# Kernel optimization log

Hardware: AMD Instinct MI355X
Metric: run time of the kernel (lower is better)

The kernel has to match this reference:

```python
import jax, jax.numpy as jnp
import numpy as np

BOUND = 1.0
N_RAYS = 2048
TOT = 128        # num_steps (samples per pixel)
IND_S = 16       # indicator_steps
MAX_DEPTHS = 2
HID = 64
EPS = 1e-8


def setup_inputs() -> dict:
    key = jax.random.key(0)
    ks = jax.random.split(key, 13)
    M = N_RAYS * TOT
    rays_o = 0.3 * jax.random.normal(ks[0], (N_RAYS, 3), jnp.float32)
    rd = jax.random.normal(ks[1], (N_RAYS, 3), jnp.float32)
    rays_d = rd / (jnp.linalg.norm(rd, axis=-1, keepdims=True) + EPS)
    env_map = 0.1 * jax.random.normal(ks[2], (3, 128, 256), jnp.float32)
    Wd1 = jax.random.normal(ks[3], (3, HID), jnp.float32) / np.sqrt(3.0)
    Wd2 = jax.random.normal(ks[4], (HID, 3), jnp.float32) / np.sqrt(HID)
    Wf1 = jax.random.normal(ks[5], (6, HID), jnp.float32) / np.sqrt(6.0)
    Ws = jax.random.normal(ks[6], (HID, 3), jnp.float32) / np.sqrt(HID)
    Wdir = jax.random.normal(ks[7], (HID, 3), jnp.float32) / np.sqrt(HID)
    Wrho = jax.random.normal(ks[8], (HID, 3), jnp.float32) / np.sqrt(HID)
    jitter = jax.random.uniform(ks[9], (MAX_DEPTHS, M, IND_S), jnp.float32)
    u_t = jax.random.uniform(ks[10], (MAX_DEPTHS, M), jnp.float32)
    u_scatter = jax.random.uniform(ks[11], (MAX_DEPTHS, M), jnp.float32)
    channel = jax.random.randint(ks[12], (MAX_DEPTHS, M), 0, 3)
    return dict(rays_o=rays_o, rays_d=rays_d, env_map=env_map, Wd1=Wd1, Wd2=Wd2,
                Wf1=Wf1, Ws=Ws, Wdir=Wdir, Wrho=Wrho,
                jitter=jitter, u_t=u_t, u_scatter=u_scatter, channel=channel)


def _density(pts, Wd1, Wd2):
    # stand-in NeRF density field: 3 spectral channels, positive
    return jax.nn.softplus(jnp.sin(pts @ Wd1) @ Wd2)


def _material(o, d, Wf1, Ws, Wdir, Wrho):
    f = jnp.tanh(jnp.concatenate([o, d], axis=-1) @ Wf1)
    sigma_t = jax.nn.softplus(f @ Ws)                     # [M,3]
    dn = f @ Wdir
    d_out = dn / (jnp.linalg.norm(dn, axis=-1, keepdims=True) + EPS)
    fused_rho = jax.nn.sigmoid(f @ Wrho)                  # [M,3]
    return sigma_t, d_out, fused_rho


def _sample_env(env_map, p):
    # equirectangular lookup == torch grid_sample(bilinear, align_corners=False, zero pad)
    x, y, z = p[:, 0], p[:, 1], p[:, 2]
    theta = jnp.nan_to_num(jnp.arctan2(x, -z)) / jnp.pi            # grid x in [-1,1]
    phi = 2.0 / jnp.pi * jnp.nan_to_num(jnp.arccos(y)) - 1.0       # grid y in [-1,1]
    C, H, W = env_map.shape
    ix = ((theta + 1.0) * W - 1.0) * 0.5
    iy = ((phi + 1.0) * H - 1.0) * 0.5
    x0 = jnp.floor(ix); y0 = jnp.floor(iy)
    wx = ix - x0; wy = iy - y0

    def tap(xc, yc, w):
        inb = (xc >= 0) & (xc < W) & (yc >= 0) & (yc < H)
        xi = jnp.clip(xc, 0, W - 1).astype(jnp.int32)
        yi = jnp.clip(yc, 0, H - 1).astype(jnp.int32)
        return (w * inb)[:, None] * env_map[:, yi, xi].T   # [M,3]

    v = (tap(x0, y0, (1 - wx) * (1 - wy)) + tap(x0 + 1, y0, wx * (1 - wy)) +
         tap(x0, y0 + 1, (1 - wx) * wy) + tap(x0 + 1, y0 + 1, wx * wy))
    return jnp.exp(v)


def _render(rays_o, rays_d, env_map, Wd1, Wd2, Wf1, Ws, Wdir, Wrho,
            jitter, u_t, u_scatter, channel):
    M = N_RAYS * TOT
    o = jnp.repeat(rays_o, TOT, axis=0)   # [M,3]
    d = jnp.repeat(rays_d, TOT, axis=0)
    alive = jnp.ones((M,), bool)          # masked version of boolean compaction
    thr = jnp.ones((M, 3), jnp.float32)
    rgbs = jnp.zeros((M, 3), jnp.float32)
    lin = jnp.linspace(0.0, 1.0, IND_S)

    for dep in range(MAX_DEPTHS):
        # ray-sphere intersection (radius=bound)
        a = jnp.sum(d * d, -1)
        b = 2.0 * jnp.sum(d * o, -1)
        c = jnp.sum(o * o, -1) - BOUND ** 2
        delta = b * b - 4.0 * a * c
        alive = alive & (delta > 0.0)
        sq = jnp.sqrt(jnp.maximum(delta, 0.0))
        nears = jnp.maximum((-b - sq) / (2.0 * a), 0.001)
        fars = jnp.maximum((-b + sq) / (2.0 * a), 0.001)
        span = fars - nears

        # stratified indicator samples -> per-channel majorant
        z = nears[:, None] + span[:, None] * lin[None, :]
        z = z + (jitter[dep] - 0.5) * (span[:, None] / IND_S)
        pts = o[:, None, :] + d[:, None, :] * z[:, :, None]          # [M,S,3]
        sigma = _density(pts.reshape(-1, 3), Wd1, Wd2).reshape(M, IND_S, 3)
        ch = channel[dep]
        maj_multi = jnp.maximum(sigma.max(axis=1), 0.001)            # [M,3]
        sig_ch = jnp.take_along_axis(sigma, ch[:, None, None], axis=2)[..., 0]
        maj = jnp.maximum(sig_ch.max(axis=1), 0.001)                 # [M]

        # free-flight sampling (last depth forces hit at far boundary)
        if dep < MAX_DEPTHS - 1:
            t = -jnp.log1p(-u_t[dep]) / maj + nears
        else:
            t = fars
        hit = alive & (t >= fars)

        # environment hit contribution
        denom = jnp.exp(-maj_multi * span[:, None]) / (maj_multi.max(-1, keepdims=True) + EPS) + EPS
        Le = _sample_env(env_map, o + d * fars[:, None])
        contrib = thr * (denom / jax.lax.stop_gradient(denom.mean(-1, keepdims=True))) * Le
        rgbs = rgbs + jnp.where(hit[:, None], contrib, 0.0)
        alive = alive & ~hit
        if dep == MAX_DEPTHS - 1:
            break

        # throughput update + null/real scattering (delta tracking)
        trans = jnp.exp(-maj_multi * (t - nears)[:, None]) / maj_multi.max(-1, keepdims=True)
        den2 = jax.lax.stop_gradient((maj_multi * trans).mean(-1, keepdims=True))
        thr = jnp.where(alive[:, None], thr * trans / den2, thr)
        o = jnp.where(alive[:, None], jax.lax.stop_gradient(o + d * t[:, None]), o)
        sigma_t, d_out, fused_rho = _material(o, d, Wf1, Ws, Wdir, Wrho)
        sp = jnp.minimum(jnp.take_along_axis(sigma_t, ch[:, None], axis=1)[:, 0] / maj, 1.0)
        sm = alive & (u_scatter[dep] < sp)
        d = jnp.where(sm[:, None], d_out, d)
        thr = jnp.where(sm[:, None], thr / (sp[:, None] + EPS) * fused_rho,
              jnp.where(alive[:, None], thr / (1.0 - sp[:, None] + EPS), thr))

    return rgbs.reshape(N_RAYS, TOT, 3).mean(axis=1)   # [N,3]


def reference(rays_o, rays_d, env_map, Wd1, Wd2, Wf1, Ws, Wdir, Wrho,
              jitter, u_t, u_scatter, channel):
    return _render(rays_o, rays_d, env_map, Wd1, Wd2, Wf1, Ws, Wdir, Wrho,
                   jitter, u_t, u_scatter, channel)
```

## Files before the change

### kernel.cpp

```cpp
#include <hip/hip_runtime.h>
#include <math.h>

#define NRAYS 2048
#define TOT   128
#define INDS  16
#define HID   64
#define EPSF  1e-8f
#define MTOT  (NRAYS*TOT)
#define NTAB  128

typedef float f32x2 __attribute__((ext_vector_type(2)));
typedef float f32x4 __attribute__((ext_vector_type(4)));

__device__ __forceinline__ float softplus_f(float x) {
    return fmaxf(x, 0.0f) + __logf(1.0f + __expf(-fabsf(x)));
}
__device__ __forceinline__ float sigmoid_f(float x) {
    return 1.0f / (1.0f + __expf(-x));
}
__device__ __forceinline__ float tanh_fast(float x) {
    float e2 = __expf(2.0f * x);
    return 1.0f - 2.0f / (e2 + 1.0f);
}
__device__ __forceinline__ f32x2 pkmax(f32x2 a, f32x2 b) {
    f32x2 r; r.x = fmaxf(a.x, b.x); r.y = fmaxf(a.y, b.y); return r;
}
__device__ __forceinline__ f32x2 pkfma(f32x2 a, f32x2 b, f32x2 c) {
    return __builtin_elementwise_fma(a, b, c);
}
__device__ __forceinline__ f32x4 fma4(f32x4 a, f32x4 b, f32x4 c) {
    return __builtin_elementwise_fma(a, b, c);
}

#define CK(i) ((float)(i)*(1.0f/15.0f) - 0.03125f)

#define MAKE_Z(jA, jB, kbase, nears, span)                                    \
    float s16 = (span) * (1.0f/16.0f);                                        \
    f32x2 z01, z23, z45, z67;                                                 \
    z01.x = fmaf((jA).x, s16, fmaf(span, CK((kbase)+0), nears));              \
    z01.y = fmaf((jA).y, s16, fmaf(span, CK((kbase)+1), nears));              \
    z23.x = fmaf((jA).z, s16, fmaf(span, CK((kbase)+2), nears));              \
    z23.y = fmaf((jA).w, s16, fmaf(span, CK((kbase)+3), nears));              \
    z45.x = fmaf((jB).x, s16, fmaf(span, CK((kbase)+4), nears));              \
    z45.y = fmaf((jB).y, s16, fmaf(span, CK((kbase)+5), nears));              \
    z67.x = fmaf((jB).z, s16, fmaf(span, CK((kbase)+6), nears));              \
    z67.y = fmaf((jB).w, s16, fmaf(span, CK((kbase)+7), nears));

#define TAB_EVAL(zz, mx0, mx1, mx2)                                           \
    {                                                                         \
        float x = ((zz) - ztab0) * invh;                                      \
        x = fminf(fmaxf(x, 0.0f), (float)(NTAB-1) - 1e-3f);                   \
        int i = (int)x; float w = x - (float)i;                               \
        f32x4 Ta = sTab[i]; f32x4 Tb = sTab[i+1];                             \
        f32x4 wv = {w, w, w, w};                                              \
        f32x4 F = fma4(wv, Tb - Ta, Ta);                                      \
        mx0 = fmaxf(mx0, F.x); mx1 = fmaxf(mx1, F.y); mx2 = fmaxf(mx2, F.z);  \
    }

#define DENSITY_J_BODY(A2, B2, W0, W1, W2v)                                   \
    {                                                                         \
        f32x2 g01 = pkfma(z01, (B2), (A2));                                   \
        f32x2 g23 = pkfma(z23, (B2), (A2));                                   \
        f32x2 g45 = pkfma(z45, (B2), (A2));                                   \
        f32x2 g67 = pkfma(z67, (B2), (A2));                                   \
        f32x2 h01, h23, h45, h67;                                             \
        h01.x = __builtin_amdgcn_sinf(g01.x); h01.y = __builtin_amdgcn_sinf(g01.y); \
        h23.x = __builtin_amdgcn_sinf(g23.x); h23.y = __builtin_amdgcn_sinf(g23.y); \
        h45.x = __builtin_amdgcn_sinf(g45.x); h45.y = __builtin_amdgcn_sinf(g45.y); \
        h67.x = __builtin_amdgcn_sinf(g67.x); h67.y = __builtin_amdgcn_sinf(g67.y); \
        a0_01 = pkfma(h01,(W0),a0_01); a0_23 = pkfma(h23,(W0),a0_23);         \
        a0_45 = pkfma(h45,(W0),a0_45); a0_67 = pkfma(h67,(W0),a0_67);         \
        a1_01 = pkfma(h01,(W1),a1_01); a1_23 = pkfma(h23,(W1),a1_23);         \
        a1_45 = pkfma(h45,(W1),a1_45); a1_67 = pkfma(h67,(W1),a1_67);         \
        a2_01 = pkfma(h01,(W2v),a2_01); a2_23 = pkfma(h23,(W2v),a2_23);       \
        a2_45 = pkfma(h45,(W2v),a2_45); a2_67 = pkfma(h67,(W2v),a2_67);       \
    }

__device__ __forceinline__ void density_max3_half_d1(
    const f32x4* __restrict__ sPW, const f32x4* __restrict__ sW01,
    const f32x2* __restrict__ sW2,
    float ox, float oy, float oz, float dx, float dy, float dz,
    float nears, float span, float4 jA, float4 jB, int kbase,
    float& mx0o, float& mx1o, float& mx2o)
{
    MAKE_Z(jA, jB, kbase, nears, span)
    f32x2 a0_01 = {0.f,0.f}, a0_23 = {0.f,0.f}, a0_45 = {0.f,0.f}, a0_67 = {0.f,0.f};
    f32x2 a1_01 = {0.f,0.f}, a1_23 = {0.f,0.f}, a1_45 = {0.f,0.f}, a1_67 = {0.f,0.f};
    f32x2 a2_01 = {0.f,0.f}, a2_23 = {0.f,0.f}, a2_45 = {0.f,0.f}, a2_67 = {0.f,0.f};
    #pragma unroll 2
    for (int j = 0; j < HID; ++j) {
        f32x4 pw  = sPW[j];
        f32x4 w01 = sW01[j];
        f32x2 w2  = sW2[j];
        float A = fmaf(ox, pw.x, fmaf(oy, pw.y, oz*pw.z));
        float B = fmaf(dx, pw.x, fmaf(dy, pw.y, dz*pw.z));
        f32x2 A2 = {A, A}, B2 = {B, B};
        f32x2 W0 = {w01.x, w01.y}, W1 = {w01.z, w01.w};
        DENSITY_J_BODY(A2, B2, W0, W1, w2)
    }
    f32x2 p0 = pkmax(pkmax(a0_01, a0_23), pkmax(a0_45, a0_67));
    f32x2 p1 = pkmax(pkmax(a1_01, a1_23), pkmax(a1_45, a1_67));
    f32x2 p2 = pkmax(pkmax(a2_01, a2_23), pkmax(a2_45, a2_67));
    mx0o = fmaxf(p0.x, p0.y);
    mx1o = fmaxf(p1.x, p1.y);
    mx2o = fmaxf(p2.x, p2.y);
}

__device__ __forceinline__ void env_logv(
    const float* __restrict__ env_map,
    float px, float py, float pz,
    float& v0, float& v1, float& v2)
{
    float theta = atan2f(px, -pz) * (1.0f/3.14159265358979323846f);
    float acv = (fabsf(py) <= 1.0f) ? acosf(py) : 0.0f;
    float phi = 0.63661977236758134308f * acv - 1.0f;
    float ixf = ((theta + 1.0f)*256.0f - 1.0f)*0.5f;
    float iyf = ((phi   + 1.0f)*128.0f - 1.0f)*0.5f;
    float x0f = floorf(ixf), y0f = floorf(iyf);
    float wx = ixf - x0f, wy = iyf - y0f;
    v0 = 0.f; v1 = 0.f; v2 = 0.f;
    auto tap = [&](float xc, float yc, float w) {
        if (xc >= 0.0f && xc < 256.0f && yc >= 0.0f && yc < 128.0f) {
            int xi = (int)xc, yi = (int)yc;
            const float* e = env_map + yi*256 + xi;
            v0 += w * e[0];
            v1 += w * e[128*256];
            v2 += w * e[2*128*256];
        }
    };
    tap(x0f,      y0f,      (1.0f-wx)*(1.0f-wy));
    tap(x0f+1.0f, y0f,      wx*(1.0f-wy));
    tap(x0f,      y0f+1.0f, (1.0f-wx)*wy);
    tap(x0f+1.0f, y0f+1.0f, wx*wy);
}

__global__ __launch_bounds__(256)
void render_kernel(const float* __restrict__ rays_o,
                   const float* __restrict__ rays_d,
                   const float* __restrict__ env_map,
                   const float* __restrict__ Wd1,
                   const float* __restrict__ Wd2,
                   const float* __restrict__ Wf1,
                   const float* __restrict__ Ws,
                   const float* __restrict__ Wdir,
                   const float* __restrict__ Wrho,
                   const float* __restrict__ jitter,
                   const float* __restrict__ u_t,
                   const float* __restrict__ u_scatter,
                   const int*   __restrict__ channel,
                   float* __restrict__ out)
{
    const int ray  = blockIdx.x;
    const int tid  = threadIdx.x;
    const int s    = tid >> 1;
    const int half = tid & 1;
    const int m    = ray * TOT + s;
    const int kbase = half * 8;

    __shared__ f32x4 sAB[HID];
    __shared__ f32x4 sW01[HID];
    __shared__ f32x2 sW2[HID];
    __shared__ f32x4 sPW[HID];
    __shared__ f32x4 sM0[HID];
    __shared__ f32x4 sM1[HID];
    __shared__ f32x4 sM2[HID];
    __shared__ f32x4 sTab[NTAB];
    __shared__ f32x4 sP0[TOT];
    __shared__ f32x4 sP1[TOT];
    __shared__ f32x2 sP2[TOT];
    __shared__ float sEnvE[3];
    __shared__ int   sCnt;
    __shared__ float sred[4][3];

    const float4* j0p = (const float4*)(jitter + (size_t)m*INDS + kbase);
    const float4* j1p = (const float4*)(jitter + ((size_t)MTOT + m)*INDS + kbase);
    float4 j0A = j0p[0], j0B = j0p[1];
    float4 j1A = j1p[0], j1B = j1p[1];
    int   ch = channel[m];
    float ut = u_t[m];
    float us = u_scatter[m];

    float ox = rays_o[ray*3+0], oy = rays_o[ray*3+1], oz = rays_o[ray*3+2];
    float dx = rays_d[ray*3+0], dy = rays_d[ray*3+1], dz = rays_d[ray*3+2];

    if (tid == 0) sCnt = 0;
    if (tid < HID) {
        const float INV2PI = 0.15915494309189535f;
        float w1x = Wd1[tid], w1y = Wd1[HID+tid], w1z = Wd1[2*HID+tid];
        float pw1x = w1x*INV2PI, pw1y = w1y*INV2PI, pw1z = w1z*INV2PI;
        float A = ox*pw1x + oy*pw1y + oz*pw1z;
        float B = dx*pw1x + dy*pw1y + dz*pw1z;
        float w20 = Wd2[3*tid], w21 = Wd2[3*tid+1], w22 = Wd2[3*tid+2];
        sAB[tid]  = (f32x4){A, A, B, B};
        sW01[tid] = (f32x4){w20, w20, w21, w21};
        sW2[tid]  = (f32x2){w22, w22};
        sPW[tid]  = (f32x4){pw1x, pw1y, pw1z, 0.0f};
        float f0 = Wf1[tid],       f1 = Wf1[HID+tid],   f2 = Wf1[2*HID+tid];
        float f3 = Wf1[3*HID+tid], f4 = Wf1[4*HID+tid], f5 = Wf1[5*HID+tid];
        float P = ox*f0 + oy*f1 + oz*f2 + dx*f3 + dy*f4 + dz*f5;
        float Q = dx*f0 + dy*f1 + dz*f2;
        sM0[tid] = (f32x4){P, Q, Ws[3*tid], Ws[3*tid+1]};
        sM1[tid] = (f32x4){Ws[3*tid+2], Wdir[3*tid], Wdir[3*tid+1], Wdir[3*tid+2]};
        sM2[tid] = (f32x4){Wrho[3*tid], Wrho[3*tid+1], Wrho[3*tid+2], 0.0f};
    }
    __syncthreads();

    float a0g = dx*dx + dy*dy + dz*dz;
    float b0g = 2.0f*(dx*ox + dy*oy + dz*oz);
    float c0g = (ox*ox + oy*oy + oz*oz) - 1.0f;
    float delta0 = b0g*b0g - 4.0f*a0g*c0g;
    bool alive = (delta0 > 0.0f);

    float nears = 0.f, fars = 0.f, span = 0.f, ztab0 = 0.f, invh = 0.f;
    if (alive) {
        float sq = sqrtf(delta0);
        nears = fmaxf((-b0g - sq) / (2.0f*a0g), 0.001f);
        fars  = fmaxf((-b0g + sq) / (2.0f*a0g), 0.001f);
        span  = fars - nears;
        ztab0 = fmaf(-span, 0.03125f, nears);
        float width = span * 1.0625f;
        float hstep = width * (1.0f/(NTAB-1));
        invh = (float)(NTAB-1) / width;
        int p = tid >> 1;
        float zp = fmaf((float)p, hstep, ztab0);
        float f0 = 0.f, f1 = 0.f, f2 = 0.f;
        const int jb = half * 32;
        #pragma unroll 4
        for (int j = jb; j < jb + 32; ++j) {
            f32x4 ab  = sAB[j];
            f32x4 w01 = sW01[j];
            f32x2 w2  = sW2[j];
            float hv = __builtin_amdgcn_sinf(fmaf(zp, ab.z, ab.x));
            f0 = fmaf(hv, w01.x, f0);
            f1 = fmaf(hv, w01.z, f1);
            f2 = fmaf(hv, w2.x, f2);
        }
        f0 += __shfl_xor(f0, 1, 64);
        f1 += __shfl_xor(f1, 1, 64);
        f2 += __shfl_xor(f2, 1, 64);
        if (half == 0) sTab[p] = (f32x4){f0, f1, f2, 0.0f};
        if (tid == 0) {
            float v0,v1,v2;
            env_logv(env_map, fmaf(dx,fars,ox), fmaf(dy,fars,oy), fmaf(dz,fars,oz),
                     v0,v1,v2);
            sEnvE[0] = __expf(v0); sEnvE[1] = __expf(v1); sEnvE[2] = __expf(v2);
        }
    }
    __syncthreads();

    float thr0 = 1.f, thr1 = 1.f, thr2 = 1.f;
    float rgb0 = 0.f, rgb1 = 0.f, rgb2 = 0.f;
    bool  tab_d1 = false;
    float tadv = 0.f;

    if (alive) {
        MAKE_Z(j0A, j0B, kbase, nears, span)
        float mx0 = -1e30f, mx1 = -1e30f, mx2 = -1e30f;
        TAB_EVAL(z01.x, mx0,mx1,mx2) TAB_EVAL(z01.y, mx0,mx1,mx2)
        TAB_EVAL(z23.x, mx0,mx1,mx2) TAB_EVAL(z23.y, mx0,mx1,mx2)
        TAB_EVAL(z45.x, mx0,mx1,mx2) TAB_EVAL(z45.y, mx0,mx1,mx2)
        TAB_EVAL(z67.x, mx0,mx1,mx2) TAB_EVAL(z67.y, mx0,mx1,mx2)
        mx0 = fmaxf(mx0, __shfl_xor(mx0, 1, 64));
        mx1 = fmaxf(mx1, __shfl_xor(mx1, 1, 64));
        mx2 = fmaxf(mx2, __shfl_xor(mx2, 1, 64));

        float maj0 = fmaxf(softplus_f(mx0), 0.001f);
        float maj1 = fmaxf(softplus_f(mx1), 0.001f);
        float maj2 = fmaxf(softplus_f(mx2), 0.001f);
        float mmax = fmaxf(fmaxf(maj0, maj1), maj2);

        float maj = (ch == 0) ? maj0 : ((ch == 1) ? maj1 : maj2);
        float t   = -log1pf(-ut) / maj + nears;

        if (t >= fars) {
            float den0 = __expf(-maj0*span)/(mmax+EPSF) + EPSF;
            float den1 = __expf(-maj1*span)/(mmax+EPSF) + EPSF;
            float den2 = __expf(-maj2*span)/(mmax+EPSF) + EPSF;
            float idm = 3.0f / (den0+den1+den2);
            rgb0 = den0*idm*sEnvE[0];
            rgb1 = den1*idm*sEnvE[1];
            rgb2 = den2*idm*sEnvE[2];
        } else {
            float tn  = t - nears;
            float imm = 1.0f / mmax;
            float tr0 = __expf(-maj0*tn) * imm;
            float tr1 = __expf(-maj1*tn) * imm;
            float tr2 = __expf(-maj2*tn) * imm;
            float i2m = 3.0f / (maj0*tr0 + maj1*tr1 + maj2*tr2);
            thr0 = tr0 * i2m;
            thr1 = tr1 * i2m;
            thr2 = tr2 * i2m;
            ox = fmaf(dx, t, ox); oy = fmaf(dy, t, oy); oz = fmaf(dz, t, oz);

            float st0=0.f, st1=0.f, st2=0.f;
            float dn0=0.f, dn1=0.f, dn2v=0.f;
            float rh0=0.f, rh1=0.f, rh2=0.f;
            const int j0 = half * 32;
            #pragma unroll 2
            for (int j = j0; j < j0 + 32; ++j) {
                f32x4 q0 = sM0[j];
                f32x4 q1 = sM1[j];
                f32x4 q2 = sM2[j];
                float pre = fmaf(t, q0.y, q0.x);
                float f = tanh_fast(pre);
                st0  = fmaf(f, q0.z, st0);
                st1  = fmaf(f, q0.w, st1);
                st2  = fmaf(f, q1.x, st2);
                dn0  = fmaf(f, q1.y, dn0);
                dn1  = fmaf(f, q1.z, dn1);
                dn2v = fmaf(f, q1.w, dn2v);
                rh0  = fmaf(f, q2.x, rh0);
                rh1  = fmaf(f, q2.y, rh1);
                rh2  = fmaf(f, q2.z, rh2);
            }
            st0  += __shfl_xor(st0, 1, 64);
            st1  += __shfl_xor(st1, 1, 64);
            st2  += __shfl_xor(st2, 1, 64);
            dn0  += __shfl_xor(dn0, 1, 64);
            dn1  += __shfl_xor(dn1, 1, 64);
            dn2v += __shfl_xor(dn2v, 1, 64);
            rh0  += __shfl_xor(rh0, 1, 64);
            rh1  += __shfl_xor(rh1, 1, 64);
            rh2  += __shfl_xor(rh2, 1, 64);

            float stch = (ch == 0) ? st0 : ((ch == 1) ? st1 : st2);
            float sp = fminf(softplus_f(stch) / maj, 1.0f);
            if (us < sp) {
                float inr = 1.0f / (sqrtf(dn0*dn0 + dn1*dn1 + dn2v*dn2v) + EPSF);
                float ndx = dn0*inr, ndy = dn1*inr, ndz = dn2v*inr;
                float isp = 1.0f/(sp + EPSF);
                float t0 = thr0 * isp * sigmoid_f(rh0);
                float t1 = thr1 * isp * sigmoid_f(rh1);
                float t2 = thr2 * isp * sigmoid_f(rh2);
                if (half == 0) {
                    int sl = atomicAdd(&sCnt, 1);
                    sP0[sl] = (f32x4){ox, oy, oz, ndx};
                    sP1[sl] = (f32x4){ndy, ndz, t0, t1};
                    sP2[sl] = (f32x2){t2, (float)m};
                }
            } else {
                float iv = 1.0f/(1.0f - sp + EPSF);
                thr0 *= iv; thr1 *= iv; thr2 *= iv;
                tab_d1 = true;
                tadv = t;
            }
        }
    }
    __syncthreads();
    int npool = sCnt;

    if (tab_d1) {
        float a1 = dx*dx + dy*dy + dz*dz;
        float b1 = 2.0f*(dx*ox + dy*oy + dz*oz);
        float c1 = (ox*ox + oy*oy + oz*oz) - 1.0f;
        float delta1 = b1*b1 - 4.0f*a1*c1;
        if (delta1 > 0.0f) {
            float sq1    = sqrtf(delta1);
            float nears1 = fmaxf((-b1 - sq1) / (2.0f*a1), 0.001f);
            float fars1  = fmaxf((-b1 + sq1) / (2.0f*a1), 0.001f);
            float span1  = fars1 - nears1;
            MAKE_Z(j1A, j1B, kbase, nears1, span1)
            float mx0 = -1e30f, mx1 = -1e30f, mx2 = -1e30f;
            TAB_EVAL(tadv + z01.x, mx0,mx1,mx2) TAB_EVAL(tadv + z01.y, mx0,mx1,mx2)
            TAB_EVAL(tadv + z23.x, mx0,mx1,mx2) TAB_EVAL(tadv + z23.y, mx0,mx1,mx2)
            TAB_EVAL(tadv + z45.x, mx0,mx1,mx2) TAB_EVAL(tadv + z45.y, mx0,mx1,mx2)
            TAB_EVAL(tadv + z67.x, mx0,mx1,mx2) TAB_EVAL(tadv + z67.y, mx0,mx1,mx2)
            mx0 = fmaxf(mx0, __shfl_xor(mx0, 1, 64));
            mx1 = fmaxf(mx1, __shfl_xor(mx1, 1, 64));
            mx2 = fmaxf(mx2, __shfl_xor(mx2, 1, 64));

            float maj0 = fmaxf(softplus_f(mx0), 0.001f);
            float maj1 = fmaxf(softplus_f(mx1), 0.001f);
            float maj2 = fmaxf(softplus_f(mx2), 0.001f);
            float mmax = fmaxf(fmaxf(maj0, maj1), maj2);

            float den0 = __expf(-maj0*span1)/(mmax+EPSF) + EPSF;
            float den1 = __expf(-maj1*span1)/(mmax+EPSF) + EPSF;
            float den2 = __expf(-maj2*span1)/(mmax+EPSF) + EPSF;
            float idm = 3.0f / (den0+den1+den2);
            rgb0 += thr0 * den0*idm*sEnvE[0];
            rgb1 += thr1 * den1*idm*sEnvE[1];
            rgb2 += thr2 * den2*idm*sEnvE[2];
        }
    }

    {
        int q = tid >> 1;
        if (q < npool) {
            f32x4 p0 = sP0[q];
            f32x4 p1 = sP1[q];
            f32x2 p2 = sP2[q];
            float pox = p0.x, poy = p0.y, poz = p0.z;
            float pdx = p0.w, pdy = p1.x, pdz = p1.y;
            float pt0 = p1.z, pt1 = p1.w, pt2 = p2.x;
            int   mm  = (int)p2.y;
            const float4* jp = (const float4*)(jitter + ((size_t)MTOT + mm)*INDS + kbase);
            float4 jA = jp[0], jB = jp[1];

            float a1 = pdx*pdx + pdy*pdy + pdz*pdz;
            float b1 = 2.0f*(pdx*pox + pdy*poy + pdz*poz);
            float c1 = (pox*pox + poy*poy + poz*poz) - 1.0f;
            float delta1 = b1*b1 - 4.0f*a1*c1;
            if (delta1 > 0.0f) {
                float sq1    = sqrtf(delta1);
                float nears1 = fmaxf((-b1 - sq1) / (2.0f*a1), 0.001f);
                float fars1  = fmaxf((-b1 + sq1) / (2.0f*a1), 0.001f);
                float span1  = fars1 - nears1;

                float mx0, mx1, mx2;
                density_max3_half_d1(sPW, sW01, sW2, pox,poy,poz, pdx,pdy,pdz,
                                     nears1, span1, jA, jB, kbase, mx0,mx1,mx2);
                mx0 = fmaxf(mx0, __shfl_xor(mx0, 1, 64));
                mx1 = fmaxf(mx1, __shfl_xor(mx1, 1, 64));
                mx2 = fmaxf(mx2, __shfl_xor(mx2, 1, 64));

                float maj0 = fmaxf(softplus_f(mx0), 0.001f);
                float maj1 = fmaxf(softplus_f(mx1), 0.001f);
                float maj2 = fmaxf(softplus_f(mx2), 0.001f);
                float mmax = fmaxf(fmaxf(maj0, maj1), maj2);

                float den0 = __expf(-maj0*span1)/(mmax+EPSF) + EPSF;
                float den1 = __expf(-maj1*span1)/(mmax+EPSF) + EPSF;
                float den2 = __expf(-maj2*span1)/(mmax+EPSF) + EPSF;
                float idm = 3.0f / (den0+den1+den2);
                float v0,v1,v2;
                env_logv(env_map, fmaf(pdx,fars1,pox), fmaf(pdy,fars1,poy),
                         fmaf(pdz,fars1,poz), v0,v1,v2);
                rgb0 += pt0 * den0*idm*__expf(v0);
                rgb1 += pt1 * den1*idm*__expf(v1);
                rgb2 += pt2 * den2*idm*__expf(v2);
            }
        }
    }

    float r0 = rgb0, r1 = rgb1, r2 = rgb2;
    #pragma unroll
    for (int off = 32; off > 0; off >>= 1) {
        r0 += __shfl_down(r0, off, 64);
        r1 += __shfl_down(r1, off, 64);
        r2 += __shfl_down(r2, off, 64);
    }
    int wave = tid >> 6;
    if ((tid & 63) == 0) {
        sred[wave][0] = r0; sred[wave][1] = r1; sred[wave][2] = r2;
    }
    __syncthreads();
    if (tid == 0) {
        out[ray*3+0] = (sred[0][0]+sred[1][0]+sred[2][0]+sred[3][0]) * (1.0f/256.0f);
        out[ray*3+1] = (sred[0][1]+sred[1][1]+sred[2][1]+sred[3][1]) * (1.0f/256.0f);
        out[ray*3+2] = (sred[0][2]+sred[1][2]+sred[2][2]+sred[3][2]) * (1.0f/256.0f);
    }
}

extern "C" void kernel_launch(void* const* d_in, const int* in_sizes, int n_in,
                              void* d_out, int out_size, void* d_ws, size_t ws_size,
                              hipStream_t stream) {
    const float* rays_o    = (const float*)d_in[0];
    const float* rays_d    = (const float*)d_in[1];
    const float* env_map   = (const float*)d_in[2];
    const float* Wd1       = (const float*)d_in[3];
    const float* Wd2       = (const float*)d_in[4];
    const float* Wf1       = (const float*)d_in[5];
    const float* Ws        = (const float*)d_in[6];
    const float* Wdir      = (const float*)d_in[7];
    const float* Wrho      = (const float*)d_in[8];
    const float* jitter    = (const float*)d_in[9];
    const float* u_t       = (const float*)d_in[10];
    const float* u_scatter = (const float*)d_in[11];
    const int*   channel   = (const int*)d_in[12];
    float* out = (float*)d_out;

    render_kernel<<<dim3(NRAYS), dim3(256), 0, stream>>>(
        rays_o, rays_d, env_map, Wd1, Wd2, Wf1, Ws, Wdir, Wrho,
        jitter, u_t, u_scatter, channel, out);
}
```

Before: 168.1 us.

## Split pooled depth-1 density eval across four lanes per sample with strided loop

The pooled second-bounce density evaluation now assigns each compacted sample to four lanes, each handling four indicator steps instead of eight. A strided loop covers the whole pool, and a second xor-shuffle stage combines the four partial maxima. The depth-1 jitter load moves inside the branch that needs it, so rays that miss the sphere skip it. This shortens the serial sine and FMA chain per lane and balances work across the block. The cost is more shuffles, duplicated env lookups across lanes, and loop overhead when the pool exceeds 64 samples.

New measurement: 168.3 us. Within noise of the previous version (+0.2%).

```diff
diff --git a/kernel.cpp b/kernel.cpp
--- a/kernel.cpp
+++ b/kernel.cpp
@@ -56,55 +56,6 @@
         f32x4 F = fma4(wv, Tb - Ta, Ta);                                      \
         mx0 = fmaxf(mx0, F.x); mx1 = fmaxf(mx1, F.y); mx2 = fmaxf(mx2, F.z);  \
     }
-
-#define DENSITY_J_BODY(A2, B2, W0, W1, W2v)                                   \
-    {                                                                         \
-        f32x2 g01 = pkfma(z01, (B2), (A2));                                   \
-        f32x2 g23 = pkfma(z23, (B2), (A2));                                   \
-        f32x2 g45 = pkfma(z45, (B2), (A2));                                   \
-        f32x2 g67 = pkfma(z67, (B2), (A2));                                   \
-        f32x2 h01, h23, h45, h67;                                             \
-        h01.x = __builtin_amdgcn_sinf(g01.x); h01.y = __builtin_amdgcn_sinf(g01.y); \
-        h23.x = __builtin_amdgcn_sinf(g23.x); h23.y = __builtin_amdgcn_sinf(g23.y); \
-        h45.x = __builtin_amdgcn_sinf(g45.x); h45.y = __builtin_amdgcn_sinf(g45.y); \
-        h67.x = __builtin_amdgcn_sinf(g67.x); h67.y = __builtin_amdgcn_sinf(g67.y); \
-        a0_01 = pkfma(h01,(W0),a0_01); a0_23 = pkfma(h23,(W0),a0_23);         \
-        a0_45 = pkfma(h45,(W0),a0_45); a0_67 = pkfma(h67,(W0),a0_67);         \
-        a1_01 = pkfma(h01,(W1),a1_01); a1_23 = pkfma(h23,(W1),a1_23);         \
-        a1_45 = pkfma(h45,(W1),a1_45); a1_67 = pkfma(h67,(W1),a1_67);         \
-        a2_01 = pkfma(h01,(W2v),a2_01); a2_23 = pkfma(h23,(W2v),a2_23);       \
-        a2_45 = pkfma(h45,(W2v),a2_45); a2_67 = pkfma(h67,(W2v),a2_67);       \
-    }
-
-__device__ __forceinline__ void density_max3_half_d1(
-    const f32x4* __restrict__ sPW, const f32x4* __restrict__ sW01,
-    const f32x2* __restrict__ sW2,
-    float ox, float oy, float oz, float dx, float dy, float dz,
-    float nears, float span, float4 jA, float4 jB, int kbase,
-    float& mx0o, float& mx1o, float& mx2o)
-{
-    MAKE_Z(jA, jB, kbase, nears, span)
-    f32x2 a0_01 = {0.f,0.f}, a0_23 = {0.f,0.f}, a0_45 = {0.f,0.f}, a0_67 = {0.f,0.f};
-    f32x2 a1_01 = {0.f,0.f}, a1_23 = {0.f,0.f}, a1_45 = {0.f,0.f}, a1_67 = {0.f,0.f};
-    f32x2 a2_01 = {0.f,0.f}, a2_23 = {0.f,0.f}, a2_45 = {0.f,0.f}, a2_67 = {0.f,0.f};
-    #pragma unroll 2
-    for (int j = 0; j < HID; ++j) {
-        f32x4 pw  = sPW[j];
-        f32x4 w01 = sW01[j];
-        f32x2 w2  = sW2[j];
-        float A = fmaf(ox, pw.x, fmaf(oy, pw.y, oz*pw.z));
-        float B = fmaf(dx, pw.x, fmaf(dy, pw.y, dz*pw.z));
-        f32x2 A2 = {A, A}, B2 = {B, B};
-        f32x2 W0 = {w01.x, w01.y}, W1 = {w01.z, w01.w};
-        DENSITY_J_BODY(A2, B2, W0, W1, w2)
-    }
-    f32x2 p0 = pkmax(pkmax(a0_01, a0_23), pkmax(a0_45, a0_67));
-    f32x2 p1 = pkmax(pkmax(a1_01, a1_23), pkmax(a1_45, a1_67));
-    f32x2 p2 = pkmax(pkmax(a2_01, a2_23), pkmax(a2_45, a2_67));
-    mx0o = fmaxf(p0.x, p0.y);
-    mx1o = fmaxf(p1.x, p1.y);
-    mx2o = fmaxf(p2.x, p2.y);
-}
 
 __device__ __forceinline__ void env_logv(
     const float* __restrict__ env_map,
@@ -173,9 +124,7 @@
     __shared__ float sred[4][3];
 
     const float4* j0p = (const float4*)(jitter + (size_t)m*INDS + kbase);
-    const float4* j1p = (const float4*)(jitter + ((size_t)MTOT + m)*INDS + kbase);
     float4 j0A = j0p[0], j0B = j0p[1];
-    float4 j1A = j1p[0], j1B = j1p[1];
     int   ch = channel[m];
     float ut = u_t[m];
     float us = u_scatter[m];
@@ -355,6 +304,8 @@
         float c1 = (ox*ox + oy*oy + oz*oz) - 1.0f;
         float delta1 = b1*b1 - 4.0f*a1*c1;
         if (delta1 > 0.0f) {
+            const float4* j1p = (const float4*)(jitter + ((size_t)MTOT + m)*INDS + kbase);
+            float4 j1A = j1p[0], j1B = j1p[1];
             float sq1    = sqrtf(delta1);
             float nears1 = fmaxf((-b1 - sq1) / (2.0f*a1), 0.001f);
             float fars1  = fmaxf((-b1 + sq1) / (2.0f*a1), 0.001f);
@@ -385,8 +336,10 @@
     }
 
     {
-        int q = tid >> 1;
-        if (q < npool) {
+        const int qlane = tid & 3;
+        const int kq    = qlane * 4;
+        const float kqf = (float)kq;
+        for (int q = tid >> 2; q < npool; q += 64) {
             f32x4 p0 = sP0[q];
             f32x4 p1 = sP1[q];
             f32x2 p2 = sP2[q];
@@ -394,25 +347,58 @@
             float pdx = p0.w, pdy = p1.x, pdz = p1.y;
             float pt0 = p1.z, pt1 = p1.w, pt2 = p2.x;
             int   mm  = (int)p2.y;
-            const float4* jp = (const float4*)(jitter + ((size_t)MTOT + mm)*INDS + kbase);
-            float4 jA = jp[0], jB = jp[1];
 
             float a1 = pdx*pdx + pdy*pdy + pdz*pdz;
             float b1 = 2.0f*(pdx*pox + pdy*poy + pdz*poz);
             float c1 = (pox*pox + poy*poy + poz*poz) - 1.0f;
             float delta1 = b1*b1 - 4.0f*a1*c1;
             if (delta1 > 0.0f) {
+                const float4* jp = (const float4*)(jitter + ((size_t)MTOT + mm)*INDS + kq);
+                float4 jq = jp[0];
                 float sq1    = sqrtf(delta1);
                 float nears1 = fmaxf((-b1 - sq1) / (2.0f*a1), 0.001f);
                 float fars1  = fmaxf((-b1 + sq1) / (2.0f*a1), 0.001f);
                 float span1  = fars1 - nears1;
-
-                float mx0, mx1, mx2;
-                density_max3_half_d1(sPW, sW01, sW2, pox,poy,poz, pdx,pdy,pdz,
-                                     nears1, span1, jA, jB, kbase, mx0,mx1,mx2);
+                float s16q   = span1 * (1.0f/16.0f);
+                f32x2 zA, zB;
+                zA.x = fmaf(jq.x, s16q, fmaf(span1, (kqf+0.0f)*(1.0f/15.0f) - 0.03125f, nears1));
+                zA.y = fmaf(jq.y, s16q, fmaf(span1, (kqf+1.0f)*(1.0f/15.0f) - 0.03125f, nears1));
+                zB.x = fmaf(jq.z, s16q, fmaf(span1, (kqf+2.0f)*(1.0f/15.0f) - 0.03125f, nears1));
+                zB.y = fmaf(jq.w, s16q, fmaf(span1, (kqf+3.0f)*(1.0f/15.0f) - 0.03125f, nears1));
+
+                f32x2 a0A = {0.f,0.f}, a0B = {0.f,0.f};
+                f32x2 a1A = {0.f,0.f}, a1B = {0.f,0.f};
+                f32x2 a2A = {0.f,0.f}, a2B = {0.f,0.f};
+                #pragma unroll 2
+                for (int j = 0; j < HID; ++j) {
+                    f32x4 pw  = sPW[j];
+                    f32x4 w01 = sW01[j];
+                    f32x2 w2  = sW2[j];
+                    float A = fmaf(pox, pw.x, fmaf(poy, pw.y, poz*pw.z));
+                    float B = fmaf(pdx, pw.x, fmaf(pdy, pw.y, pdz*pw.z));
+                    f32x2 A2 = {A, A}, B2 = {B, B};
+                    f32x2 gA = pkfma(zA, B2, A2);
+                    f32x2 gB = pkfma(zB, B2, A2);
+                    f32x2 hA, hB;
+                    hA.x = __builtin_amdgcn_sinf(gA.x); hA.y = __builtin_amdgcn_sinf(gA.y);
+                    hB.x = __builtin_amdgcn_sinf(gB.x); hB.y = __builtin_amdgcn_sinf(gB.y);
+                    f32x2 W0 = {w01.x, w01.y}, W1 = {w01.z, w01.w};
+                    a0A = pkfma(hA, W0, a0A); a0B = pkfma(hB, W0, a0B);
+                    a1A = pkfma(hA, W1, a1A); a1B = pkfma(hB, W1, a1B);
+                    a2A = pkfma(hA, w2, a2A); a2B = pkfma(hB, w2, a2B);
+                }
+                f32x2 pm0 = pkmax(a0A, a0B);
+                f32x2 pm1 = pkmax(a1A, a1B);
+                f32x2 pm2 = pkmax(a2A, a2B);
+                float mx0 = fmaxf(pm0.x, pm0.y);
+                float mx1 = fmaxf(pm1.x, pm1.y);
+                float mx2 = fmaxf(pm2.x, pm2.y);
                 mx0 = fmaxf(mx0, __shfl_xor(mx0, 1, 64));
                 mx1 = fmaxf(mx1, __shfl_xor(mx1, 1, 64));
                 mx2 = fmaxf(mx2, __shfl_xor(mx2, 1, 64));
+                mx0 = fmaxf(mx0, __shfl_xor(mx0, 2, 64));
+                mx1 = fmaxf(mx1, __shfl_xor(mx1, 2, 64));
+                mx2 = fmaxf(mx2, __shfl_xor(mx2, 2, 64));
 
                 float maj0 = fmaxf(softplus_f(mx0), 0.001f);
                 float maj1 = fmaxf(softplus_f(mx1), 0.001f);
@@ -426,9 +412,11 @@
                 float v0,v1,v2;
                 env_logv(env_map, fmaf(pdx,fars1,pox), fmaf(pdy,fars1,poy),
                          fmaf(pdz,fars1,poz), v0,v1,v2);
-                rgb0 += pt0 * den0*idm*__expf(v0);
-                rgb1 += pt1 * den1*idm*__expf(v1);
-                rgb2 += pt2 * den2*idm*__expf(v2);
+                if (qlane < 2) {
+                    rgb0 += pt0 * den0*idm*__expf(v0);
+                    rgb1 += pt1 * den1*idm*__expf(v1);
+                    rgb2 += pt2 * den2*idm*__expf(v2);
+                }
             }
         }
     }
```
